# Kernel optimization log

Hardware: AMD Instinct MI355X
Metric: run time of the kernel (lower is better)

## Reference

```python
import jax, jax.numpy as jnp
import numpy as np


def setup_inputs() -> dict:
    key = jax.random.key(0)
    k1, k2, k3, k4 = jax.random.split(key, 4)
    B, T_dec, T_enc, H2 = 8, 64, 512, 512  # H2 = 2*hiddenSize
    encoderOutput = jax.random.normal(k1, (B, T_enc, H2), dtype=jnp.float32)
    decoderInput = jax.random.normal(k2, (B, T_dec, H2), dtype=jnp.float32)
    # fc: Linear(4H -> 2H); torch weight layout [out, in] = [2H, 4H]
    W = jax.random.normal(k3, (H2, 2 * H2), dtype=jnp.float32) * (1.0 / np.sqrt(2 * H2))
    b = jax.random.normal(k4, (H2,), dtype=jnp.float32) * 0.01
    return {"encoderOutput": encoderOutput, "decoderInput": decoderInput, "W": W, "b": b}


def reference(encoderOutput, decoderInput, W, b):
    # Original: for each (i, j), fc(cat(dec[:,i], enc[:,j])) then log_softmax over
    # the FEATURE dim (dim=1 of the flattened [-1, 2H] tensor), then
    # context[:, i] = sum_j log_softmax(...) * enc[:, j].
    H2 = encoderOutput.shape[-1]
    W_dec = W[:, :H2]   # columns multiplying the decoder half of the concat
    W_enc = W[:, H2:]   # columns multiplying the encoder half
    dec_part = jnp.einsum('bid,od->bio', decoderInput, W_dec)   # [B, T_dec, 2H]
    enc_part = jnp.einsum('bjd,od->bjo', encoderOutput, W_enc)  # [B, T_enc, 2H]
    logits = dec_part[:, :, None, :] + enc_part[:, None, :, :] + b  # [B, T_dec, T_enc, 2H]
    alpha = jax.nn.log_softmax(logits, axis=-1)  # softmax over feature dim, as in source
    context = jnp.einsum('bijd,bjd->bid', alpha, encoderOutput)  # [B, T_dec, 2H]
    return context
```

## Files before the change

kernel.cpp:

```cpp
#include <hip/hip_runtime.h>


namespace {
constexpr int kH  = 512;
constexpr int kTD = 64;
constexpr int kTE = 512;
constexpr int kB  = 8;
constexpr int kRD = kB * kTD;
constexpr int kRE = kB * kTE;
}

typedef __attribute__((ext_vector_type(8))) short short8;
typedef __attribute__((ext_vector_type(4))) float floatx4;

__device__ __forceinline__ unsigned short f2bf(float x) {
    unsigned u = __float_as_uint(x);
    u += 0x7fffu + ((u >> 16) & 1u);
    return (unsigned short)(u >> 16);
}
__device__ __forceinline__ float bf2f(unsigned short h) {
    return __uint_as_float(((unsigned)h) << 16);
}
__device__ __forceinline__ size_t fragTile(int rtile, int kt) {
    return ((size_t)rtile * 16 + kt) * 512;
}
__device__ __forceinline__ short8 pack8(float4 a, float4 b) {
    short8 r;
    r[0] = (short)f2bf(a.x); r[1] = (short)f2bf(a.y);
    r[2] = (short)f2bf(a.z); r[3] = (short)f2bf(a.w);
    r[4] = (short)f2bf(b.x); r[5] = (short)f2bf(b.y);
    r[6] = (short)f2bf(b.z); r[7] = (short)f2bf(b.w);
    return r;
}

__global__ __launch_bounds__(256) void fused_cast(
    const float* __restrict__ W, const float* __restrict__ dec,
    const float* __restrict__ enc,
    unsigned short* __restrict__ Wd_f, unsigned short* __restrict__ We_f,
    unsigned short* __restrict__ dec_f,
    unsigned short* __restrict__ enc_f, unsigned short* __restrict__ encT_f,
    float* __restrict__ S12)
{
    const int blk = blockIdx.x, t = threadIdx.x;
    const int w = t >> 6, l = t & 63;
    const int lr = l & 15, lc = l >> 4;
    if (blk < 256) {
        const int gw = blk * 4 + w;
        const int sel = gw >> 9, rem = gw & 511;
        const int ot = rem >> 4, kt = rem & 15;
        const int o = ot * 16 + lr;
        const float* src = W + (size_t)o * 1024 + sel * 512 + kt * 32 + lc * 8;
        const float4 v0 = *(const float4*)src;
        const float4 v1 = *(const float4*)(src + 4);
        unsigned short* dst = (sel ? We_f : Wd_f) + fragTile(ot, kt) + l * 8;
        *(short8*)dst = pack8(v0, v1);
        if (blk < 32) S12[blk * 256 + t] = 0.f;
    } else if (blk < 384) {
        const int gw = (blk - 256) * 4 + w;
        const int rt = gw >> 4, kt = gw & 15;
        const int r = rt * 16 + lr;
        const float* src = dec + (size_t)r * kH + kt * 32 + lc * 8;
        const float4 v0 = *(const float4*)src;
        const float4 v1 = *(const float4*)(src + 4);
        *(short8*)(dec_f + fragTile(rt, kt) + l * 8) = pack8(v0, v1);
    } else {
        __shared__ unsigned short s[64][36];
        const int e = blk - 384;
        const int kt = e & 15, jt = (e >> 4) & 7, b = e >> 7;
        const int j0 = jt * 64, d0 = kt * 32;
        const int jl = w * 16 + lr;
        const float* src = enc + ((size_t)(b * kTE + j0 + jl)) * kH + d0 + lc * 8;
        const float4 v0 = *(const float4*)src;
        const float4 v1 = *(const float4*)(src + 4);
        const short8 p = pack8(v0, v1);
        *(short8*)(enc_f + fragTile(b * 32 + jt * 4 + w, kt) + l * 8) = p;
#pragma unroll
        for (int i = 0; i < 8; ++i) s[jl][lc * 8 + i] = (unsigned short)p[i];
        __syncthreads();
        const int dt = w >> 1, jc = w & 1;
        const int dl = dt * 16 + lr;
        const int j8 = jc * 32 + lc * 8;
        short8 v;
#pragma unroll
        for (int i = 0; i < 8; ++i) v[i] = (short)s[j8 + i][dl];
        *(short8*)(encT_f + fragTile(b * 32 + kt * 2 + dt, jt * 2 + jc) + l * 8) = v;
    }
}

__global__ __launch_bounds__(256) void gemm1(
    const unsigned short* __restrict__ enc_f,
    const unsigned short* __restrict__ dec_f,
    const unsigned short* __restrict__ Wd_f,
    const unsigned short* __restrict__ We_f,
    const float* __restrict__ bias,
    const float* __restrict__ enc,
    unsigned short* __restrict__ part_bf, unsigned short* __restrict__ uv_f,
    float* __restrict__ S12)
{
    __shared__ float As[64][68];
    __shared__ float r1[16][68];
    __shared__ float r2[16][68];
    const int tile = blockIdx.x;
    const int ns = tile & 7, ms = tile >> 3;
    const int t = threadIdx.x, w = t >> 6, l = t & 63;
    const int qm = w >> 1, qn = w & 1;
    const bool isenc = (ms >= 8);
    const unsigned short* A = isenc ? enc_f : dec_f;
    const unsigned short* Bw = isenc ? We_f : Wd_f;
    const int art = (isenc ? (ms - 8) : ms) * 4 + qm * 2;
    const int brt = ns * 4 + qn * 2;

    floatx4 acc[2][2];
#pragma unroll
    for (int m = 0; m < 2; ++m)
#pragma unroll
        for (int n = 0; n < 2; ++n) acc[m][n] = (floatx4){0.f, 0.f, 0.f, 0.f};

    for (int kt = 0; kt < 16; ++kt) {
        short8 af[2], bfr[2];
#pragma unroll
        for (int m = 0; m < 2; ++m)
            af[m] = *(const short8*)(A + fragTile(art + m, kt) + l * 8);
#pragma unroll
        for (int n = 0; n < 2; ++n)
            bfr[n] = *(const short8*)(Bw + fragTile(brt + n, kt) + l * 8);
#pragma unroll
        for (int m = 0; m < 2; ++m)
#pragma unroll
            for (int n = 0; n < 2; ++n)
                acc[m][n] = __builtin_amdgcn_mfma_f32_16x16x32_bf16(af[m], bfr[n], acc[m][n], 0, 0, 0);
    }

    const int lr = l & 15, lq = l >> 4;
#pragma unroll
    for (int m = 0; m < 2; ++m)
#pragma unroll
        for (int n = 0; n < 2; ++n)
#pragma unroll
            for (int r = 0; r < 4; ++r)
                As[qm * 32 + m * 16 + lq * 4 + r][qn * 32 + n * 16 + lr] = acc[m][n][r];
    __syncthreads();

    const int rowbase = ms * 64, colbase = ns * 64;
    if (!isenc) {
#pragma unroll
        for (int h = 0; h < 2; ++h) {
            const int a = h * 256 + t;
            const int row = a >> 3, cc = (a & 7) * 8;
            const float4 v0 = *(const float4*)&As[row][cc];
            const float4 v1 = *(const float4*)&As[row][cc + 4];
            *(short8*)(part_bf + (size_t)(rowbase + row) * kH + colbase + cc) = pack8(v0, v1);
        }
    }
#pragma unroll
    for (int h = 0; h < 2; ++h) {
        const int s = h * 256 + t;
        const int rt = s >> 7, kc = (s >> 6) & 1, fl = s & 63;
        const int row = rt * 16 + (fl & 15);
        const int col = kc * 32 + (fl >> 4) * 8;
        const float4 v0 = *(const float4*)&As[row][col];
        const float4 v1 = *(const float4*)&As[row][col + 4];
        float4 b0 = make_float4(0.f, 0.f, 0.f, 0.f), b1 = b0;
        if (isenc) {
            b0 = *(const float4*)(bias + colbase + col);
            b1 = *(const float4*)(bias + colbase + col + 4);
        }
        short8 u;
        u[0] = (short)f2bf(__expf(v0.x + b0.x));
        u[1] = (short)f2bf(__expf(v0.y + b0.y));
        u[2] = (short)f2bf(__expf(v0.z + b0.z));
        u[3] = (short)f2bf(__expf(v0.w + b0.w));
        u[4] = (short)f2bf(__expf(v1.x + b1.x));
        u[5] = (short)f2bf(__expf(v1.y + b1.y));
        u[6] = (short)f2bf(__expf(v1.z + b1.z));
        u[7] = (short)f2bf(__expf(v1.w + b1.w));
        *(short8*)(uv_f + fragTile(ms * 4 + rt, ns * 2 + kc) + fl * 8) = u;
    }
    if (isenc) {
        const int b = (ms - 8) >> 3;
        const int jbase = ((ms - 8) & 7) * 64;
        const int o4 = (t & 15) * 4, jg = t >> 4;
        float4 s1p = make_float4(0.f, 0.f, 0.f, 0.f);
        float4 s2p = make_float4(0.f, 0.f, 0.f, 0.f);
#pragma unroll
        for (int jj = 0; jj < 4; ++jj) {
            const int j = jg * 4 + jj;
            const float4 ev = *(const float4*)(
                enc + ((size_t)(b * kTE + jbase + j)) * kH + colbase + o4);
            const float4 pv = *(const float4*)&As[j][o4];
            s1p.x += ev.x; s1p.y += ev.y; s1p.z += ev.z; s1p.w += ev.w;
            s2p.x = fmaf(pv.x, ev.x, s2p.x);
            s2p.y = fmaf(pv.y, ev.y, s2p.y);
            s2p.z = fmaf(pv.z, ev.z, s2p.z);
            s2p.w = fmaf(pv.w, ev.w, s2p.w);
        }
        *(float4*)&r1[jg][o4] = s1p;
        *(float4*)&r2[jg][o4] = s2p;
        __syncthreads();
        if (t < 64) {
            float a1 = 0.f, a2 = 0.f;
#pragma unroll
            for (int g = 0; g < 16; ++g) { a1 += r1[g][t]; a2 += r2[g][t]; }
            atomicAdd(&S12[b * kH + colbase + t], a1);
            atomicAdd(&S12[4096 + b * kH + colbase + t], a2);
        }
    }
}

__global__ __launch_bounds__(256) void lse_k(
    const unsigned short* __restrict__ uv_f, unsigned short* __restrict__ lse_f)
{
    __shared__ float red[4][16][68];
    const int blk = blockIdx.x, t = threadIdx.x;
    const int b = blk >> 5, rem = blk & 31;
    const int it = rem >> 3, jt = rem & 7;
    const int w = t >> 6, l = t & 63;
    const int art = b * 4 + it;
    const int vrt0 = 32 + b * 32 + jt * 4;

    floatx4 acc[4];
#pragma unroll
    for (int n = 0; n < 4; ++n) acc[n] = (floatx4){0.f, 0.f, 0.f, 0.f};
#pragma unroll
    for (int kk = 0; kk < 4; ++kk) {
        const int kt = w * 4 + kk;
        const short8 af = *(const short8*)(uv_f + fragTile(art, kt) + l * 8);
#pragma unroll
        for (int n = 0; n < 4; ++n)
            acc[n] = __builtin_amdgcn_mfma_f32_16x16x32_bf16(
                af, *(const short8*)(uv_f + fragTile(vrt0 + n, kt) + l * 8), acc[n], 0, 0, 0);
    }
    const int lr = l & 15, lq = l >> 4;
#pragma unroll
    for (int n = 0; n < 4; ++n)
#pragma unroll
        for (int r = 0; r < 4; ++r)
            red[w][lq * 4 + r][n * 16 + lr] = acc[n][r];
    __syncthreads();
    const int s = t >> 1, h = t & 1;
    const int kc = s >> 6, fl = s & 63;
    const int i = fl & 15;
    const int j = kc * 32 + (fl >> 4) * 8 + h * 4;
    float4 sum = *(const float4*)&red[0][i][j];
    const float4 s1 = *(const float4*)&red[1][i][j];
    const float4 s2 = *(const float4*)&red[2][i][j];
    const float4 s3 = *(const float4*)&red[3][i][j];
    sum.x += s1.x + s2.x + s3.x; sum.y += s1.y + s2.y + s3.y;
    sum.z += s1.z + s2.z + s3.z; sum.w += s1.w + s2.w + s3.w;
    ushort4 o;
    o.x = f2bf(__logf(sum.x)); o.y = f2bf(__logf(sum.y));
    o.z = f2bf(__logf(sum.z)); o.w = f2bf(__logf(sum.w));
    *(ushort4*)(lse_f + fragTile(b * 4 + it, jt * 2 + kc) + fl * 8 + h * 4) = o;
}

__global__ __launch_bounds__(256) void final_k(
    const unsigned short* __restrict__ lse_f,
    const unsigned short* __restrict__ encT_f,
    const unsigned short* __restrict__ part_bf,
    const float* __restrict__ bias,
    const float* __restrict__ S12,
    float* __restrict__ out)
{
    __shared__ float red[4][16][68];
    const int blk = blockIdx.x, t = threadIdx.x;
    const int b = blk >> 5, rem = blk & 31;
    const int it = rem >> 3, dt = rem & 7;
    const int w = t >> 6, l = t & 63;
    const int art = b * 4 + it;
    const int brt0 = b * 32 + dt * 4;

    floatx4 acc[4];
#pragma unroll
    for (int n = 0; n < 4; ++n) acc[n] = (floatx4){0.f, 0.f, 0.f, 0.f};
#pragma unroll
    for (int kk = 0; kk < 4; ++kk) {
        const int kt = w * 4 + kk;
        const short8 af = *(const short8*)(lse_f + fragTile(art, kt) + l * 8);
#pragma unroll
        for (int n = 0; n < 4; ++n)
            acc[n] = __builtin_amdgcn_mfma_f32_16x16x32_bf16(
                af, *(const short8*)(encT_f + fragTile(brt0 + n, kt) + l * 8), acc[n], 0, 0, 0);
    }
    const int lr = l & 15, lq = l >> 4;
#pragma unroll
    for (int n = 0; n < 4; ++n)
#pragma unroll
        for (int r = 0; r < 4; ++r)
            red[w][lq * 4 + r][n * 16 + lr] = acc[n][r];
    __syncthreads();
    const int i = t >> 4, d0 = (t & 15) * 4;
    float4 m = *(const float4*)&red[0][i][d0];
    const float4 m1 = *(const float4*)&red[1][i][d0];
    const float4 m2 = *(const float4*)&red[2][i][d0];
    const float4 m3 = *(const float4*)&red[3][i][d0];
    m.x += m1.x + m2.x + m3.x; m.y += m1.y + m2.y + m3.y;
    m.z += m1.z + m2.z + m3.z; m.w += m1.w + m2.w + m3.w;

    const int gd = dt * 64 + d0;
    const float4 s1 = *(const float4*)(S12 + b * kH + gd);
    const float4 s2 = *(const float4*)(S12 + 4096 + b * kH + gd);
    const float4 bi = *(const float4*)(bias + gd);
    const int row = b * kTD + it * 16 + i;
    const ushort4 dp = *(const ushort4*)(part_bf + (size_t)row * kH + gd);
    float4 o;
    o.x = fmaf(bf2f(dp.x) + bi.x, s1.x, s2.x) - m.x;
    o.y = fmaf(bf2f(dp.y) + bi.y, s1.y, s2.y) - m.y;
    o.z = fmaf(bf2f(dp.z) + bi.z, s1.z, s2.z) - m.z;
    o.w = fmaf(bf2f(dp.w) + bi.w, s1.w, s2.w) - m.w;
    *(float4*)(out + (size_t)row * kH + gd) = o;
}

extern "C" void kernel_launch(void* const* d_in, const int* in_sizes, int n_in,
                              void* d_out, int out_size, void* d_ws, size_t ws_size,
                              hipStream_t stream)
{
    (void)in_sizes; (void)n_in; (void)out_size; (void)ws_size;
    const float* enc  = (const float*)d_in[0];
    const float* dec  = (const float*)d_in[1];
    const float* W    = (const float*)d_in[2];
    const float* bias = (const float*)d_in[3];
    float* out = (float*)d_out;

    char* base = (char*)d_ws;
    unsigned short* part_bf = (unsigned short*)(base);
    unsigned short* uv_f    = (unsigned short*)(base + 4718592);
    unsigned short* enc_f   = (unsigned short*)(base + 9437184);
    unsigned short* encT_f  = (unsigned short*)(base + 13631488);
    unsigned short* dec_f   = (unsigned short*)(base + 17825792);
    unsigned short* Wd_f    = (unsigned short*)(base + 18350080);
    unsigned short* We_f    = (unsigned short*)(base + 18874368);
    unsigned short* lse_f   = (unsigned short*)(base + 19398656);
    float*          S12     = (float*)(base + 19922944);

    fused_cast<<<1408, 256, 0, stream>>>(W, dec, enc, Wd_f, We_f, dec_f,
                                         enc_f, encT_f, S12);
    gemm1<<<576, 256, 0, stream>>>(enc_f, dec_f, Wd_f, We_f, bias, enc,
                                   part_bf, uv_f, S12);
    lse_k<<<256, 256, 0, stream>>>(uv_f, lse_f);
    final_k<<<256, 256, 0, stream>>>(lse_f, encT_f, part_bf, bias, S12, out);
}
```

Baseline: 91.87 us.

## Merge gemm, lse and final kernels into one launch with atomic-flag dependencies

Combines the three dependent kernels into a single 1088-block launch. Producer blocks bump per-batch and per-row-tile counters with release atomics, and consumer blocks spin on them with acquire fences. This removes two kernel launch boundaries and their tail drains, and lets later stages start per batch while other batches are still computing. The cost is spin-waiting, plus a deadlock risk if consumer blocks get resident before producers. Block index order makes that unlikely.

```diff
diff --git a/kernel.cpp b/kernel.cpp
--- a/kernel.cpp
+++ b/kernel.cpp
@@ -7,7 +7,6 @@
 constexpr int kTE = 512;
 constexpr int kB  = 8;
 constexpr int kRD = kB * kTD;
-constexpr int kRE = kB * kTE;
 }
 
 typedef __attribute__((ext_vector_type(8))) short short8;
@@ -39,7 +38,7 @@
     unsigned short* __restrict__ Wd_f, unsigned short* __restrict__ We_f,
     unsigned short* __restrict__ dec_f,
     unsigned short* __restrict__ enc_f, unsigned short* __restrict__ encT_f,
-    float* __restrict__ S12)
+    float* __restrict__ S12, int* __restrict__ flags)
 {
     const int blk = blockIdx.x, t = threadIdx.x;
     const int w = t >> 6, l = t & 63;
@@ -55,6 +54,7 @@
         unsigned short* dst = (sel ? We_f : Wd_f) + fragTile(ot, kt) + l * 8;
         *(short8*)dst = pack8(v0, v1);
         if (blk < 32) S12[blk * 256 + t] = 0.f;
+        if (blk == 0 && t < 64) flags[t] = 0;
     } else if (blk < 384) {
         const int gw = (blk - 256) * 4 + w;
         const int rt = gw >> 4, kt = gw & 15;
@@ -87,7 +87,7 @@
     }
 }
 
-__global__ __launch_bounds__(256) void gemm1(
+__global__ __launch_bounds__(256) void work(
     const unsigned short* __restrict__ enc_f,
     const unsigned short* __restrict__ dec_f,
     const unsigned short* __restrict__ Wd_f,
@@ -95,219 +95,230 @@
     const float* __restrict__ bias,
     const float* __restrict__ enc,
     unsigned short* __restrict__ part_bf, unsigned short* __restrict__ uv_f,
-    float* __restrict__ S12)
-{
-    __shared__ float As[64][68];
-    __shared__ float r1[16][68];
-    __shared__ float r2[16][68];
-    const int tile = blockIdx.x;
-    const int ns = tile & 7, ms = tile >> 3;
-    const int t = threadIdx.x, w = t >> 6, l = t & 63;
-    const int qm = w >> 1, qn = w & 1;
-    const bool isenc = (ms >= 8);
-    const unsigned short* A = isenc ? enc_f : dec_f;
-    const unsigned short* Bw = isenc ? We_f : Wd_f;
-    const int art = (isenc ? (ms - 8) : ms) * 4 + qm * 2;
-    const int brt = ns * 4 + qn * 2;
-
-    floatx4 acc[2][2];
-#pragma unroll
-    for (int m = 0; m < 2; ++m)
-#pragma unroll
-        for (int n = 0; n < 2; ++n) acc[m][n] = (floatx4){0.f, 0.f, 0.f, 0.f};
-
-    for (int kt = 0; kt < 16; ++kt) {
-        short8 af[2], bfr[2];
-#pragma unroll
-        for (int m = 0; m < 2; ++m)
-            af[m] = *(const short8*)(A + fragTile(art + m, kt) + l * 8);
-#pragma unroll
-        for (int n = 0; n < 2; ++n)
-            bfr[n] = *(const short8*)(Bw + fragTile(brt + n, kt) + l * 8);
-#pragma unroll
-        for (int m = 0; m < 2; ++m)
-#pragma unroll
-            for (int n = 0; n < 2; ++n)
-                acc[m][n] = __builtin_amdgcn_mfma_f32_16x16x32_bf16(af[m], bfr[n], acc[m][n], 0, 0, 0);
-    }
-
-    const int lr = l & 15, lq = l >> 4;
-#pragma unroll
-    for (int m = 0; m < 2; ++m)
-#pragma unroll
-        for (int n = 0; n < 2; ++n)
-#pragma unroll
-            for (int r = 0; r < 4; ++r)
-                As[qm * 32 + m * 16 + lq * 4 + r][qn * 32 + n * 16 + lr] = acc[m][n][r];
-    __syncthreads();
-
-    const int rowbase = ms * 64, colbase = ns * 64;
-    if (!isenc) {
-#pragma unroll
-        for (int h = 0; h < 2; ++h) {
-            const int a = h * 256 + t;
-            const int row = a >> 3, cc = (a & 7) * 8;
-            const float4 v0 = *(const float4*)&As[row][cc];
-            const float4 v1 = *(const float4*)&As[row][cc + 4];
-            *(short8*)(part_bf + (size_t)(rowbase + row) * kH + colbase + cc) = pack8(v0, v1);
-        }
-    }
-#pragma unroll
-    for (int h = 0; h < 2; ++h) {
-        const int s = h * 256 + t;
-        const int rt = s >> 7, kc = (s >> 6) & 1, fl = s & 63;
-        const int row = rt * 16 + (fl & 15);
-        const int col = kc * 32 + (fl >> 4) * 8;
-        const float4 v0 = *(const float4*)&As[row][col];
-        const float4 v1 = *(const float4*)&As[row][col + 4];
-        float4 b0 = make_float4(0.f, 0.f, 0.f, 0.f), b1 = b0;
-        if (isenc) {
-            b0 = *(const float4*)(bias + colbase + col);
-            b1 = *(const float4*)(bias + colbase + col + 4);
-        }
-        short8 u;
-        u[0] = (short)f2bf(__expf(v0.x + b0.x));
-        u[1] = (short)f2bf(__expf(v0.y + b0.y));
-        u[2] = (short)f2bf(__expf(v0.z + b0.z));
-        u[3] = (short)f2bf(__expf(v0.w + b0.w));
-        u[4] = (short)f2bf(__expf(v1.x + b1.x));
-        u[5] = (short)f2bf(__expf(v1.y + b1.y));
-        u[6] = (short)f2bf(__expf(v1.z + b1.z));
-        u[7] = (short)f2bf(__expf(v1.w + b1.w));
-        *(short8*)(uv_f + fragTile(ms * 4 + rt, ns * 2 + kc) + fl * 8) = u;
-    }
-    if (isenc) {
-        const int b = (ms - 8) >> 3;
-        const int jbase = ((ms - 8) & 7) * 64;
-        const int o4 = (t & 15) * 4, jg = t >> 4;
-        float4 s1p = make_float4(0.f, 0.f, 0.f, 0.f);
-        float4 s2p = make_float4(0.f, 0.f, 0.f, 0.f);
-#pragma unroll
-        for (int jj = 0; jj < 4; ++jj) {
-            const int j = jg * 4 + jj;
-            const float4 ev = *(const float4*)(
-                enc + ((size_t)(b * kTE + jbase + j)) * kH + colbase + o4);
-            const float4 pv = *(const float4*)&As[j][o4];
-            s1p.x += ev.x; s1p.y += ev.y; s1p.z += ev.z; s1p.w += ev.w;
-            s2p.x = fmaf(pv.x, ev.x, s2p.x);
-            s2p.y = fmaf(pv.y, ev.y, s2p.y);
-            s2p.z = fmaf(pv.z, ev.z, s2p.z);
-            s2p.w = fmaf(pv.w, ev.w, s2p.w);
-        }
-        *(float4*)&r1[jg][o4] = s1p;
-        *(float4*)&r2[jg][o4] = s2p;
-        __syncthreads();
-        if (t < 64) {
-            float a1 = 0.f, a2 = 0.f;
-#pragma unroll
-            for (int g = 0; g < 16; ++g) { a1 += r1[g][t]; a2 += r2[g][t]; }
-            atomicAdd(&S12[b * kH + colbase + t], a1);
-            atomicAdd(&S12[4096 + b * kH + colbase + t], a2);
-        }
-    }
-}
-
-__global__ __launch_bounds__(256) void lse_k(
-    const unsigned short* __restrict__ uv_f, unsigned short* __restrict__ lse_f)
-{
-    __shared__ float red[4][16][68];
-    const int blk = blockIdx.x, t = threadIdx.x;
-    const int b = blk >> 5, rem = blk & 31;
-    const int it = rem >> 3, jt = rem & 7;
-    const int w = t >> 6, l = t & 63;
-    const int art = b * 4 + it;
-    const int vrt0 = 32 + b * 32 + jt * 4;
-
-    floatx4 acc[4];
-#pragma unroll
-    for (int n = 0; n < 4; ++n) acc[n] = (floatx4){0.f, 0.f, 0.f, 0.f};
-#pragma unroll
-    for (int kk = 0; kk < 4; ++kk) {
-        const int kt = w * 4 + kk;
-        const short8 af = *(const short8*)(uv_f + fragTile(art, kt) + l * 8);
-#pragma unroll
-        for (int n = 0; n < 4; ++n)
-            acc[n] = __builtin_amdgcn_mfma_f32_16x16x32_bf16(
-                af, *(const short8*)(uv_f + fragTile(vrt0 + n, kt) + l * 8), acc[n], 0, 0, 0);
-    }
-    const int lr = l & 15, lq = l >> 4;
-#pragma unroll
-    for (int n = 0; n < 4; ++n)
-#pragma unroll
-        for (int r = 0; r < 4; ++r)
-            red[w][lq * 4 + r][n * 16 + lr] = acc[n][r];
-    __syncthreads();
-    const int s = t >> 1, h = t & 1;
-    const int kc = s >> 6, fl = s & 63;
-    const int i = fl & 15;
-    const int j = kc * 32 + (fl >> 4) * 8 + h * 4;
-    float4 sum = *(const float4*)&red[0][i][j];
-    const float4 s1 = *(const float4*)&red[1][i][j];
-    const float4 s2 = *(const float4*)&red[2][i][j];
-    const float4 s3 = *(const float4*)&red[3][i][j];
-    sum.x += s1.x + s2.x + s3.x; sum.y += s1.y + s2.y + s3.y;
-    sum.z += s1.z + s2.z + s3.z; sum.w += s1.w + s2.w + s3.w;
-    ushort4 o;
-    o.x = f2bf(__logf(sum.x)); o.y = f2bf(__logf(sum.y));
-    o.z = f2bf(__logf(sum.z)); o.w = f2bf(__logf(sum.w));
-    *(ushort4*)(lse_f + fragTile(b * 4 + it, jt * 2 + kc) + fl * 8 + h * 4) = o;
-}
-
-__global__ __launch_bounds__(256) void final_k(
-    const unsigned short* __restrict__ lse_f,
+    unsigned short* __restrict__ lse_f,
     const unsigned short* __restrict__ encT_f,
-    const unsigned short* __restrict__ part_bf,
-    const float* __restrict__ bias,
-    const float* __restrict__ S12,
+    float* __restrict__ S12, int* __restrict__ flags,
     float* __restrict__ out)
 {
-    __shared__ float red[4][16][68];
+    __shared__ __align__(16) char smem[26112];
     const int blk = blockIdx.x, t = threadIdx.x;
-    const int b = blk >> 5, rem = blk & 31;
-    const int it = rem >> 3, dt = rem & 7;
     const int w = t >> 6, l = t & 63;
-    const int art = b * 4 + it;
-    const int brt0 = b * 32 + dt * 4;
-
-    floatx4 acc[4];
-#pragma unroll
-    for (int n = 0; n < 4; ++n) acc[n] = (floatx4){0.f, 0.f, 0.f, 0.f};
-#pragma unroll
-    for (int kk = 0; kk < 4; ++kk) {
-        const int kt = w * 4 + kk;
-        const short8 af = *(const short8*)(lse_f + fragTile(art, kt) + l * 8);
+    const int lr = l & 15, lq = l >> 4;
+    int* uvcnt  = flags;
+    int* lsecnt = flags + 8;
+
+    if (blk < 576) {
+        float (*As)[68] = (float(*)[68])smem;
+        float (*r1)[68] = (float(*)[68])(smem + 17408);
+        float (*r2)[68] = (float(*)[68])(smem + 21760);
+        const int tile = blk;
+        const int ns = tile & 7, ms = tile >> 3;
+        const int qm = w >> 1, qn = w & 1;
+        const bool isenc = (ms >= 8);
+        const unsigned short* A = isenc ? enc_f : dec_f;
+        const unsigned short* Bw = isenc ? We_f : Wd_f;
+        const int art = (isenc ? (ms - 8) : ms) * 4 + qm * 2;
+        const int brt = ns * 4 + qn * 2;
+
+        floatx4 acc[2][2];
+#pragma unroll
+        for (int m = 0; m < 2; ++m)
+#pragma unroll
+            for (int n = 0; n < 2; ++n) acc[m][n] = (floatx4){0.f, 0.f, 0.f, 0.f};
+
+        for (int kt = 0; kt < 16; ++kt) {
+            short8 af[2], bfr[2];
+#pragma unroll
+            for (int m = 0; m < 2; ++m)
+                af[m] = *(const short8*)(A + fragTile(art + m, kt) + l * 8);
+#pragma unroll
+            for (int n = 0; n < 2; ++n)
+                bfr[n] = *(const short8*)(Bw + fragTile(brt + n, kt) + l * 8);
+#pragma unroll
+            for (int m = 0; m < 2; ++m)
+#pragma unroll
+                for (int n = 0; n < 2; ++n)
+                    acc[m][n] = __builtin_amdgcn_mfma_f32_16x16x32_bf16(af[m], bfr[n], acc[m][n], 0, 0, 0);
+        }
+
+#pragma unroll
+        for (int m = 0; m < 2; ++m)
+#pragma unroll
+            for (int n = 0; n < 2; ++n)
+#pragma unroll
+                for (int r = 0; r < 4; ++r)
+                    As[qm * 32 + m * 16 + lq * 4 + r][qn * 32 + n * 16 + lr] = acc[m][n][r];
+        __syncthreads();
+
+        const int rowbase = ms * 64, colbase = ns * 64;
+        if (!isenc) {
+#pragma unroll
+            for (int h = 0; h < 2; ++h) {
+                const int a = h * 256 + t;
+                const int row = a >> 3, cc = (a & 7) * 8;
+                const float4 v0 = *(const float4*)&As[row][cc];
+                const float4 v1 = *(const float4*)&As[row][cc + 4];
+                *(short8*)(part_bf + (size_t)(rowbase + row) * kH + colbase + cc) = pack8(v0, v1);
+            }
+        }
+#pragma unroll
+        for (int h = 0; h < 2; ++h) {
+            const int s = h * 256 + t;
+            const int rt = s >> 7, kc = (s >> 6) & 1, fl = s & 63;
+            const int row = rt * 16 + (fl & 15);
+            const int col = kc * 32 + (fl >> 4) * 8;
+            const float4 v0 = *(const float4*)&As[row][col];
+            const float4 v1 = *(const float4*)&As[row][col + 4];
+            float4 b0 = make_float4(0.f, 0.f, 0.f, 0.f), b1 = b0;
+            if (isenc) {
+                b0 = *(const float4*)(bias + colbase + col);
+                b1 = *(const float4*)(bias + colbase + col + 4);
+            }
+            short8 u;
+            u[0] = (short)f2bf(__expf(v0.x + b0.x));
+            u[1] = (short)f2bf(__expf(v0.y + b0.y));
+            u[2] = (short)f2bf(__expf(v0.z + b0.z));
+            u[3] = (short)f2bf(__expf(v0.w + b0.w));
+            u[4] = (short)f2bf(__expf(v1.x + b1.x));
+            u[5] = (short)f2bf(__expf(v1.y + b1.y));
+            u[6] = (short)f2bf(__expf(v1.z + b1.z));
+            u[7] = (short)f2bf(__expf(v1.w + b1.w));
+            *(short8*)(uv_f + fragTile(ms * 4 + rt, ns * 2 + kc) + fl * 8) = u;
+        }
+        if (isenc) {
+            const int b = (ms - 8) >> 3;
+            const int jbase = ((ms - 8) & 7) * 64;
+            const int o4 = (t & 15) * 4, jg = t >> 4;
+            float4 s1p = make_float4(0.f, 0.f, 0.f, 0.f);
+            float4 s2p = make_float4(0.f, 0.f, 0.f, 0.f);
+#pragma unroll
+            for (int jj = 0; jj < 4; ++jj) {
+                const int j = jg * 4 + jj;
+                const float4 ev = *(const float4*)(
+                    enc + ((size_t)(b * kTE + jbase + j)) * kH + colbase + o4);
+                const float4 pv = *(const float4*)&As[j][o4];
+                s1p.x += ev.x; s1p.y += ev.y; s1p.z += ev.z; s1p.w += ev.w;
+                s2p.x = fmaf(pv.x, ev.x, s2p.x);
+                s2p.y = fmaf(pv.y, ev.y, s2p.y);
+                s2p.z = fmaf(pv.z, ev.z, s2p.z);
+                s2p.w = fmaf(pv.w, ev.w, s2p.w);
+            }
+            *(float4*)&r1[jg][o4] = s1p;
+            *(float4*)&r2[jg][o4] = s2p;
+            __syncthreads();
+            if (t < 64) {
+                float a1 = 0.f, a2 = 0.f;
+#pragma unroll
+                for (int g = 0; g < 16; ++g) { a1 += r1[g][t]; a2 += r2[g][t]; }
+                atomicAdd(&S12[b * kH + colbase + t], a1);
+                atomicAdd(&S12[4096 + b * kH + colbase + t], a2);
+            }
+        }
+        __syncthreads();
+        if (t == 0) {
+            const int batch = isenc ? ((ms - 8) >> 3) : ms;
+            __hip_atomic_fetch_add(&uvcnt[batch], 1, __ATOMIC_RELEASE,
+                                   __HIP_MEMORY_SCOPE_AGENT);
+        }
+    } else if (blk < 832) {
+        float (*red)[16][68] = (float(*)[16][68])smem;
+        const int u = blk - 576;
+        const int b = u >> 5, rem = u & 31;
+        const int it = rem >> 3, jt = rem & 7;
+        while (__hip_atomic_load(&uvcnt[b], __ATOMIC_RELAXED,
+                                 __HIP_MEMORY_SCOPE_AGENT) < 72)
+            __builtin_amdgcn_s_sleep(2);
+        __builtin_amdgcn_fence(__ATOMIC_ACQUIRE, "agent");
+
+        const int art = b * 4 + it;
+        const int vrt0 = 32 + b * 32 + jt * 4;
+        floatx4 acc[4];
+#pragma unroll
+        for (int n = 0; n < 4; ++n) acc[n] = (floatx4){0.f, 0.f, 0.f, 0.f};
+#pragma unroll
+        for (int kk = 0; kk < 4; ++kk) {
+            const int kt = w * 4 + kk;
+            const short8 af = *(const short8*)(uv_f + fragTile(art, kt) + l * 8);
+#pragma unroll
+            for (int n = 0; n < 4; ++n)
+                acc[n] = __builtin_amdgcn_mfma_f32_16x16x32_bf16(
+                    af, *(const short8*)(uv_f + fragTile(vrt0 + n, kt) + l * 8), acc[n], 0, 0, 0);
+        }
 #pragma unroll
         for (int n = 0; n < 4; ++n)
-            acc[n] = __builtin_amdgcn_mfma_f32_16x16x32_bf16(
-                af, *(const short8*)(encT_f + fragTile(brt0 + n, kt) + l * 8), acc[n], 0, 0, 0);
+#pragma unroll
+            for (int r = 0; r < 4; ++r)
+                red[w][lq * 4 + r][n * 16 + lr] = acc[n][r];
+        __syncthreads();
+        const int s = t >> 1, h = t & 1;
+        const int kc = s >> 6, fl = s & 63;
+        const int i = fl & 15;
+        const int j = kc * 32 + (fl >> 4) * 8 + h * 4;
+        float4 sum = *(const float4*)&red[0][i][j];
+        const float4 s1 = *(const float4*)&red[1][i][j];
+        const float4 s2 = *(const float4*)&red[2][i][j];
+        const float4 s3 = *(const float4*)&red[3][i][j];
+        sum.x += s1.x + s2.x + s3.x; sum.y += s1.y + s2.y + s3.y;
+        sum.z += s1.z + s2.z + s3.z; sum.w += s1.w + s2.w + s3.w;
+        ushort4 o;
+        o.x = f2bf(__logf(sum.x)); o.y = f2bf(__logf(sum.y));
+        o.z = f2bf(__logf(sum.z)); o.w = f2bf(__logf(sum.w));
+        *(ushort4*)(lse_f + fragTile(b * 4 + it, jt * 2 + kc) + fl * 8 + h * 4) = o;
+        __syncthreads();
+        if (t == 0)
+            __hip_atomic_fetch_add(&lsecnt[b * 4 + it], 1, __ATOMIC_RELEASE,
+                                   __HIP_MEMORY_SCOPE_AGENT);
+    } else {
+        float (*red)[16][68] = (float(*)[16][68])smem;
+        const int u = blk - 832;
+        const int b = u >> 5, rem = u & 31;
+        const int it = rem >> 3, dt = rem & 7;
+        while (__hip_atomic_load(&lsecnt[b * 4 + it], __ATOMIC_RELAXED,
+                                 __HIP_MEMORY_SCOPE_AGENT) < 8)
+            __builtin_amdgcn_s_sleep(2);
+        __builtin_amdgcn_fence(__ATOMIC_ACQUIRE, "agent");
+
+        const int art = b * 4 + it;
+        const int brt0 = b * 32 + dt * 4;
+        floatx4 acc[4];
+#pragma unroll
+        for (int n = 0; n < 4; ++n) acc[n] = (floatx4){0.f, 0.f, 0.f, 0.f};
+#pragma unroll
+        for (int kk = 0; kk < 4; ++kk) {
+            const int kt = w * 4 + kk;
+            const short8 af = *(const short8*)(lse_f + fragTile(art, kt) + l * 8);
+#pragma unroll
+            for (int n = 0; n < 4; ++n)
+                acc[n] = __builtin_amdgcn_mfma_f32_16x16x32_bf16(
+                    af, *(const short8*)(encT_f + fragTile(brt0 + n, kt) + l * 8), acc[n], 0, 0, 0);
+        }
+#pragma unroll
+        for (int n = 0; n < 4; ++n)
+#pragma unroll
+            for (int r = 0; r < 4; ++r)
+                red[w][lq * 4 + r][n * 16 + lr] = acc[n][r];
+        __syncthreads();
+        const int i = t >> 4, d0 = (t & 15) * 4;
+        float4 m = *(const float4*)&red[0][i][d0];
+        const float4 m1 = *(const float4*)&red[1][i][d0];
+        const float4 m2 = *(const float4*)&red[2][i][d0];
+        const float4 m3 = *(const float4*)&red[3][i][d0];
+        m.x += m1.x + m2.x + m3.x; m.y += m1.y + m2.y + m3.y;
+        m.z += m1.z + m2.z + m3.z; m.w += m1.w + m2.w + m3.w;
+
+        const int gd = dt * 64 + d0;
+        const float4 s1 = *(const float4*)(S12 + b * kH + gd);
+        const float4 s2 = *(const float4*)(S12 + 4096 + b * kH + gd);
+        const float4 bi = *(const float4*)(bias + gd);
+        const int row = b * kTD + it * 16 + i;
+        const ushort4 dp = *(const ushort4*)(part_bf + (size_t)row * kH + gd);
+        float4 o;
+        o.x = fmaf(bf2f(dp.x) + bi.x, s1.x, s2.x) - m.x;
+        o.y = fmaf(bf2f(dp.y) + bi.y, s1.y, s2.y) - m.y;
+        o.z = fmaf(bf2f(dp.z) + bi.z, s1.z, s2.z) - m.z;
+        o.w = fmaf(bf2f(dp.w) + bi.w, s1.w, s2.w) - m.w;
+        *(float4*)(out + (size_t)row * kH + gd) = o;
     }
-    const int lr = l & 15, lq = l >> 4;
-#pragma unroll
-    for (int n = 0; n < 4; ++n)
-#pragma unroll
-        for (int r = 0; r < 4; ++r)
-            red[w][lq * 4 + r][n * 16 + lr] = acc[n][r];
-    __syncthreads();
-    const int i = t >> 4, d0 = (t & 15) * 4;
-    float4 m = *(const float4*)&red[0][i][d0];
-    const float4 m1 = *(const float4*)&red[1][i][d0];
-    const float4 m2 = *(const float4*)&red[2][i][d0];
-    const float4 m3 = *(const float4*)&red[3][i][d0];
-    m.x += m1.x + m2.x + m3.x; m.y += m1.y + m2.y + m3.y;
-    m.z += m1.z + m2.z + m3.z; m.w += m1.w + m2.w + m3.w;
-
-    const int gd = dt * 64 + d0;
-    const float4 s1 = *(const float4*)(S12 + b * kH + gd);
-    const float4 s2 = *(const float4*)(S12 + 4096 + b * kH + gd);
-    const float4 bi = *(const float4*)(bias + gd);
-    const int row = b * kTD + it * 16 + i;
-    const ushort4 dp = *(const ushort4*)(part_bf + (size_t)row * kH + gd);
-    float4 o;
-    o.x = fmaf(bf2f(dp.x) + bi.x, s1.x, s2.x) - m.x;
-    o.y = fmaf(bf2f(dp.y) + bi.y, s1.y, s2.y) - m.y;
-    o.z = fmaf(bf2f(dp.z) + bi.z, s1.z, s2.z) - m.z;
-    o.w = fmaf(bf2f(dp.w) + bi.w, s1.w, s2.w) - m.w;
-    *(float4*)(out + (size_t)row * kH + gd) = o;
 }
 
 extern "C" void kernel_launch(void* const* d_in, const int* in_sizes, int n_in,
@@ -331,11 +342,10 @@
     unsigned short* We_f    = (unsigned short*)(base + 18874368);
     unsigned short* lse_f   = (unsigned short*)(base + 19398656);
     float*          S12     = (float*)(base + 19922944);
+    int*            flags   = (int*)(base + 19955712);
 
     fused_cast<<<1408, 256, 0, stream>>>(W, dec, enc, Wd_f, We_f, dec_f,
-                                         enc_f, encT_f, S12);
-    gemm1<<<576, 256, 0, stream>>>(enc_f, dec_f, Wd_f, We_f, bias, enc,
-                                   part_bf, uv_f, S12);
-    lse_k<<<256, 256, 0, stream>>>(uv_f, lse_f);
-    final_k<<<256, 256, 0, stream>>>(lse_f, encT_f, part_bf, bias, S12, out);
-}
+                                         enc_f, encT_f, S12, flags);
+    work<<<1088, 256, 0, stream>>>(enc_f, dec_f, Wd_f, We_f, bias, enc,
+                                   part_bf, uv_f, lse_f, encT_f, S12, flags, out);
+}
```

Measured after the change: 183.1 us. 1.99x slower.

## Move encoder transpose into gemm1 extra blocks and coarsen encoder cast

Applied to the files above, without the earlier changes.

The encoder transpose-to-fragment work leaves the cast kernel and runs as 128 extra blocks appended to the gemm1 grid, each looping over 8 k-tiles through shared memory. It can then overlap with the GEMM tiles, since only final_k consumes encT_f. The remaining encoder cast blocks each handle 4 k-tiles, shrinking the cast grid. The cost is an extra shared buffer in gemm1, which may lower occupancy, and a serialized transpose loop with two barriers per iteration.

```diff
diff --git a/kernel.cpp b/kernel.cpp
--- a/kernel.cpp
+++ b/kernel.cpp
@@ -7,7 +7,6 @@
 constexpr int kTE = 512;
 constexpr int kB  = 8;
 constexpr int kRD = kB * kTD;
-constexpr int kRE = kB * kTE;
 }
 
 typedef __attribute__((ext_vector_type(8))) short short8;
@@ -37,8 +36,7 @@
     const float* __restrict__ W, const float* __restrict__ dec,
     const float* __restrict__ enc,
     unsigned short* __restrict__ Wd_f, unsigned short* __restrict__ We_f,
-    unsigned short* __restrict__ dec_f,
-    unsigned short* __restrict__ enc_f, unsigned short* __restrict__ encT_f,
+    unsigned short* __restrict__ dec_f, unsigned short* __restrict__ enc_f,
     float* __restrict__ S12)
 {
     const int blk = blockIdx.x, t = threadIdx.x;
@@ -64,26 +62,19 @@
         const float4 v1 = *(const float4*)(src + 4);
         *(short8*)(dec_f + fragTile(rt, kt) + l * 8) = pack8(v0, v1);
     } else {
-        __shared__ unsigned short s[64][36];
         const int e = blk - 384;
-        const int kt = e & 15, jt = (e >> 4) & 7, b = e >> 7;
-        const int j0 = jt * 64, d0 = kt * 32;
-        const int jl = w * 16 + lr;
-        const float* src = enc + ((size_t)(b * kTE + j0 + jl)) * kH + d0 + lc * 8;
-        const float4 v0 = *(const float4*)src;
-        const float4 v1 = *(const float4*)(src + 4);
-        const short8 p = pack8(v0, v1);
-        *(short8*)(enc_f + fragTile(b * 32 + jt * 4 + w, kt) + l * 8) = p;
-#pragma unroll
-        for (int i = 0; i < 8; ++i) s[jl][lc * 8 + i] = (unsigned short)p[i];
-        __syncthreads();
-        const int dt = w >> 1, jc = w & 1;
-        const int dl = dt * 16 + lr;
-        const int j8 = jc * 32 + lc * 8;
-        short8 v;
-#pragma unroll
-        for (int i = 0; i < 8; ++i) v[i] = (short)s[j8 + i][dl];
-        *(short8*)(encT_f + fragTile(b * 32 + kt * 2 + dt, jt * 2 + jc) + l * 8) = v;
+        const int b = e >> 5, rem = e & 31;
+        const int jt = rem >> 2, kq = rem & 3;
+        const int rtile = b * 32 + jt * 4 + w;
+        const int row = rtile * 16 + lr;
+#pragma unroll
+        for (int i = 0; i < 4; ++i) {
+            const int kt = kq * 4 + i;
+            const float* src = enc + (size_t)row * kH + kt * 32 + lc * 8;
+            const float4 v0 = *(const float4*)src;
+            const float4 v1 = *(const float4*)(src + 4);
+            *(short8*)(enc_f + fragTile(rtile, kt) + l * 8) = pack8(v0, v1);
+        }
     }
 }
 
@@ -95,14 +86,46 @@
     const float* __restrict__ bias,
     const float* __restrict__ enc,
     unsigned short* __restrict__ part_bf, unsigned short* __restrict__ uv_f,
+    unsigned short* __restrict__ encT_f,
     float* __restrict__ S12)
 {
     __shared__ float As[64][68];
     __shared__ float r1[16][68];
     __shared__ float r2[16][68];
-    const int tile = blockIdx.x;
+    __shared__ unsigned short sT[64][36];
+    const int blk = blockIdx.x, t = threadIdx.x;
+    const int w = t >> 6, l = t & 63;
+    const int lr = l & 15, lq = l >> 4, lc = l >> 4;
+
+    if (blk >= 576) {
+        const int e = blk - 576;
+        const int b = e >> 4, sub = e & 15;
+        const int jt = sub >> 1, kh = sub & 1;
+        const int j0 = jt * 64;
+        const int jl = w * 16 + lr;
+        for (int kt = kh * 8; kt < kh * 8 + 8; ++kt) {
+            const int d0 = kt * 32;
+            const float* src = enc + ((size_t)(b * kTE + j0 + jl)) * kH + d0 + lc * 8;
+            const float4 v0 = *(const float4*)src;
+            const float4 v1 = *(const float4*)(src + 4);
+            const short8 p = pack8(v0, v1);
+            __syncthreads();
+#pragma unroll
+            for (int i = 0; i < 8; ++i) sT[jl][lc * 8 + i] = (unsigned short)p[i];
+            __syncthreads();
+            const int dt2 = w >> 1, jc = w & 1;
+            const int dl = dt2 * 16 + lr;
+            const int j8 = jc * 32 + lc * 8;
+            short8 v;
+#pragma unroll
+            for (int i = 0; i < 8; ++i) v[i] = (short)sT[j8 + i][dl];
+            *(short8*)(encT_f + fragTile(b * 32 + kt * 2 + dt2, jt * 2 + jc) + l * 8) = v;
+        }
+        return;
+    }
+
+    const int tile = blk;
     const int ns = tile & 7, ms = tile >> 3;
-    const int t = threadIdx.x, w = t >> 6, l = t & 63;
     const int qm = w >> 1, qn = w & 1;
     const bool isenc = (ms >= 8);
     const unsigned short* A = isenc ? enc_f : dec_f;
@@ -131,7 +154,6 @@
                 acc[m][n] = __builtin_amdgcn_mfma_f32_16x16x32_bf16(af[m], bfr[n], acc[m][n], 0, 0, 0);
     }
 
-    const int lr = l & 15, lq = l >> 4;
 #pragma unroll
     for (int m = 0; m < 2; ++m)
 #pragma unroll
@@ -332,10 +354,10 @@
     unsigned short* lse_f   = (unsigned short*)(base + 19398656);
     float*          S12     = (float*)(base + 19922944);
 
-    fused_cast<<<1408, 256, 0, stream>>>(W, dec, enc, Wd_f, We_f, dec_f,
-                                         enc_f, encT_f, S12);
-    gemm1<<<576, 256, 0, stream>>>(enc_f, dec_f, Wd_f, We_f, bias, enc,
-                                   part_bf, uv_f, S12);
+    fused_cast<<<640, 256, 0, stream>>>(W, dec, enc, Wd_f, We_f, dec_f,
+                                        enc_f, S12);
+    gemm1<<<704, 256, 0, stream>>>(enc_f, dec_f, Wd_f, We_f, bias, enc,
+                                   part_bf, uv_f, encT_f, S12);
     lse_k<<<256, 256, 0, stream>>>(uv_f, lse_f);
     final_k<<<256, 256, 0, stream>>>(lse_f, encT_f, part_bf, bias, S12, out);
 }
```

Result: no change. 92.19 us (+0.3%).
